# Performance work log

Hardware: AMD Instinct MI355X
Metric: run time of the kernel (lower is better)

Reference implementation:

```python
import jax, jax.numpy as jnp
import numpy as np

SQ3 = 3.0 ** 0.5

# ---- Clebsch-Gordan (real-basis Wigner 3j) constants, e3nn conventions ----
# e3nn real SH basis: polar axis = y, m=-l..l, azimuthal cos->z, sin->x,
# l=1 component order (x, y, z). Tensors normalized to unit Frobenius norm
# (e3nn wigner_3j normalization); overall sign is absorbed by random weights.

def _m2_basis():
    # symmetric traceless 3x3 matrices M_k with x^T M_k x = Y2_k(x)
    M = np.zeros((5, 3, 3))
    M[0, 0, 2] = M[0, 2, 0] = SQ3 / 2          # sqrt(3) x z
    M[1, 0, 1] = M[1, 1, 0] = SQ3 / 2          # sqrt(3) x y
    M[2] = np.diag([-0.5, 1.0, -0.5])           # y^2 - (x^2+z^2)/2
    M[3, 1, 2] = M[3, 2, 1] = SQ3 / 2          # sqrt(3) y z
    M[4] = np.diag([-SQ3 / 2, 0.0, SQ3 / 2])    # (sqrt(3)/2)(z^2-x^2)
    return M

def _w3j_112():
    C = np.zeros((3, 3, 5))
    C[0, 2, 0] = C[2, 0, 0] = SQ3 / 2
    C[0, 1, 1] = C[1, 0, 1] = SQ3 / 2
    C[1, 1, 2] = 1.0; C[0, 0, 2] = -0.5; C[2, 2, 2] = -0.5
    C[1, 2, 3] = C[2, 1, 3] = SQ3 / 2
    C[2, 2, 4] = SQ3 / 2; C[0, 0, 4] = -SQ3 / 2
    return C / np.linalg.norm(C)

def _w3j_222():
    M = _m2_basis()
    C = np.zeros((5, 5, 5))
    for i in range(5):
        for j in range(5):
            P = 0.5 * (M[i] @ M[j] + M[j] @ M[i])
            P -= (np.trace(P) / 3.0) * np.eye(3)
            for k in range(5):
                C[i, j, k] = np.trace(P @ M[k]) / 1.5
    return C / np.linalg.norm(C)

W112 = jnp.asarray(_w3j_112(), dtype=jnp.float32)
W222 = jnp.asarray(_w3j_222(), dtype=jnp.float32)


def _sh_component(v):
    # e3nn spherical harmonics, normalize=False, normalization='component'
    x, y, z = v[:, 0], v[:, 1], v[:, 2]
    x2, y2, z2 = x * x, y * y, z * z
    sh1 = SQ3 * v  # [E,3]
    sh2 = (5.0 ** 0.5) * jnp.stack([
        SQ3 * x * z,
        SQ3 * x * y,
        y2 - 0.5 * (x2 + z2),
        SQ3 * y * z,
        (SQ3 / 2.0) * (z2 - x2),
    ], axis=-1)  # [E,5]
    # l=3 SH exist in irreps_sh but no tp1 instruction consumes them (mid has no l=3)
    return sh1, sh2


def _forward(x, pos, tp1_w0, tp1_w1, tp1_w2, w_0e2e, w_2e0e, w_1o1o, w_2e2e):
    N = x.shape[0]
    E = N // 2  # setup guarantees exactly N/2 True entries per mask
    from_idx = jnp.nonzero(x[:, 0] > 0.5, size=E, fill_value=0)[0]
    to_idx = jnp.nonzero(x[:, 1] > 0.5, size=E, fill_value=0)[0]
    edge_vec = pos[to_idx] - pos[from_idx]          # [E,3]
    nf = x[to_idx]                                   # [E,2]  (2x0e)
    sh1, sh2 = _sh_component(edge_vec)

    # tp1: FCTP(2x0e, sh, 64x0e+24x1e+24x1o+16x2e+16x2o).
    # Live paths: 0e x 0e -> 0e, 0e x 1o -> 1o, 0e x 2e -> 2e; each path's
    # sqrt(dim_out/2) norm coeff times w3j(0,l,l)=delta/sqrt(2l+1) nets 1/sqrt(2).
    # 1e and 2o mid channels are structurally zero.
    # Sum over edges then / sqrt(6) (num_neighbors**0.5), folded into `inv`.
    inv = 1.0 / (2.0 ** 0.5 * 6.0 ** 0.5)
    g0 = inv * jnp.sum(nf @ tp1_w0, axis=0)                   # [64]  (sh0 == 1)
    g1 = inv * jnp.einsum('ew,ej->wj', nf @ tp1_w1, sh1)      # [24,3]
    g2 = inv * jnp.einsum('ew,ej->wj', nf @ tp1_w2, sh2)      # [16,5]

    # tp2: FCTP(mid, mid, 1x2e). element path norm: alpha = 5 / sum(mul1*mul2)
    # over ALL 10 instructions targeting 2e = 5248 (dead paths still count).
    c = (5.0 / 5248.0) ** 0.5
    inv_s5 = 1.0 / 5.0 ** 0.5  # w3j(0,2,2) = delta / sqrt(5)
    out = c * (
        inv_s5 * jnp.einsum('uv,u,vk->k', w_0e2e, g0, g2)
        + inv_s5 * jnp.einsum('uv,uk,v->k', w_2e0e, g2, g0)
        + jnp.einsum('uv,ui,vj,ijk->k', w_1o1o, g1, g1, W112)
        + jnp.einsum('uv,ui,vj,ijk->k', w_2e2e, g2, g2, W222)
    )
    return out  # [5]  (1x2e)


def setup_inputs() -> dict:
    key = jax.random.key(0)
    ks = jax.random.split(key, 9)
    N = 2_000_000
    E = N // 2
    base = 0.49 * jax.random.uniform(ks[0], (N, 2), dtype=jnp.float32)
    is_from = (jnp.arange(N) < E).astype(jnp.float32)
    # first half of nodes: x[:,0] > 0.5 (edge sources); second half: x[:,1] > 0.5 (targets)
    x = base.at[:, 0].add(0.51 * is_from).at[:, 1].add(0.51 * (1.0 - is_from))
    pos = jax.random.normal(ks[1], (N, 3), dtype=jnp.float32)
    return {
        'x': x,
        'pos': pos,
        'tp1_w0': jax.random.normal(ks[2], (2, 64), dtype=jnp.float32),
        'tp1_w1': jax.random.normal(ks[3], (2, 24), dtype=jnp.float32),
        'tp1_w2': jax.random.normal(ks[4], (2, 16), dtype=jnp.float32),
        'w_0e2e': jax.random.normal(ks[5], (64, 16), dtype=jnp.float32),
        'w_2e0e': jax.random.normal(ks[6], (16, 64), dtype=jnp.float32),
        'w_1o1o': jax.random.normal(ks[7], (24, 24), dtype=jnp.float32),
        'w_2e2e': jax.random.normal(ks[8], (16, 16), dtype=jnp.float32),
    }


def reference(x, pos, tp1_w0, tp1_w1, tp1_w2, w_0e2e, w_2e0e, w_1o1o, w_2e2e):
    return _forward(x, pos, tp1_w0, tp1_w1, tp1_w2, w_0e2e, w_2e0e, w_1o1o, w_2e2e)
```

## Files before the change

### kernel.cpp

```cpp
#include <hip/hip_runtime.h>

#define SQ3F 1.7320508075688772f
#define SQ5F 2.2360679774997896f
#define BLOCK 256
#define CHUNK 2048
#define ROUNDS 8
#define EPB 1024

__device__ const float M2B[5][3][3] = {
  {{0.f, 0.f, 0.8660254037844386f}, {0.f, 0.f, 0.f}, {0.8660254037844386f, 0.f, 0.f}},
  {{0.f, 0.8660254037844386f, 0.f}, {0.8660254037844386f, 0.f, 0.f}, {0.f, 0.f, 0.f}},
  {{-0.5f, 0.f, 0.f}, {0.f, 1.0f, 0.f}, {0.f, 0.f, -0.5f}},
  {{0.f, 0.f, 0.f}, {0.f, 0.f, 0.8660254037844386f}, {0.f, 0.8660254037844386f, 0.f}},
  {{-0.8660254037844386f, 0.f, 0.f}, {0.f, 0.f, 0.f}, {0.f, 0.f, 0.8660254037844386f}}
};

__device__ __forceinline__ void accum18(float* s, float nx, float ny,
                                        float ex, float ey, float ez) {
  float x2 = ex * ex, y2 = ey * ey, z2 = ez * ez;
  float s1x = SQ3F * ex, s1y = SQ3F * ey, s1z = SQ3F * ez;
  float s20 = SQ5F * SQ3F * ex * ez;
  float s21 = SQ5F * SQ3F * ex * ey;
  float s22 = SQ5F * (y2 - 0.5f * (x2 + z2));
  float s23 = SQ5F * SQ3F * ey * ez;
  float s24 = SQ5F * 0.5f * SQ3F * (z2 - x2);
  s[0] += nx;        s[1] += ny;
  s[2] += nx * s1x;  s[3] += nx * s1y;  s[4] += nx * s1z;
  s[5] += ny * s1x;  s[6] += ny * s1y;  s[7] += ny * s1z;
  s[8]  += nx * s20; s[9]  += nx * s21; s[10] += nx * s22;
  s[11] += nx * s23; s[12] += nx * s24;
  s[13] += ny * s20; s[14] += ny * s21; s[15] += ny * s22;
  s[16] += ny * s23; s[17] += ny * s24;
}

__device__ __forceinline__ void block_reduce_store(float* s, float* dst) {
  const int t = threadIdx.x, lane = t & 63, wave = t >> 6;
#pragma unroll
  for (int j = 0; j < 18; ++j)
    for (int o = 32; o; o >>= 1) s[j] += __shfl_down(s[j], o);
  __shared__ float ls[4][18];
  if (lane == 0) {
#pragma unroll
    for (int j = 0; j < 18; ++j) ls[wave][j] = s[j];
  }
  __syncthreads();
  if (t < 18) dst[t] = ls[0][t] + ls[1][t] + ls[2][t] + ls[3][t];
}

__device__ void do_finalize(const float* accS,
                            const float* w0, const float* w1, const float* w2,
                            const float* w_0e2e, const float* w_2e0e,
                            const float* w_1o1o, const float* w_2e2e,
                            float* out) {
  const int t = threadIdx.x;
  __shared__ float g0[64], g1[24][3], g2[16][5];
  __shared__ float a16[16], c16[16], T1[24][3], T2[16][5];
  __shared__ float A1[3][3], A2[5][5];
  __shared__ float W112s[45], W222s[125];
  __shared__ float rn112, rn222;
  if (t >= 64 && t < 109) W112s[t - 64] = 0.f;
  __syncthreads();

  const float inv = 0.28867513459481287f;
  if (t < 64) {
    g0[t] = inv * (accS[0] * w0[t] + accS[1] * w0[64 + t]);
  } else if (t < 136) {
    int i2 = t - 64, w = i2 / 3, j = i2 % 3;
    g1[w][j] = inv * (accS[2 + j] * w1[w] + accS[5 + j] * w1[24 + w]);
  } else if (t < 216) {
    int i2 = t - 136, w = i2 / 5, j = i2 % 5;
    g2[w][j] = inv * (accS[8 + j] * w2[w] + accS[13 + j] * w2[16 + w]);
  } else if (t < 241) {
    int idx = t - 216, i = idx / 5, j = idx % 5;
    float P[3][3];
    for (int a = 0; a < 3; ++a)
      for (int bb = 0; bb < 3; ++bb) {
        float sacc = 0.f;
        for (int cc = 0; cc < 3; ++cc)
          sacc += M2B[i][a][cc] * M2B[j][cc][bb] + M2B[j][a][cc] * M2B[i][cc][bb];
        P[a][bb] = 0.5f * sacc;
      }
    float tr3 = (P[0][0] + P[1][1] + P[2][2]) * (1.0f / 3.0f);
    P[0][0] -= tr3; P[1][1] -= tr3; P[2][2] -= tr3;
    for (int k = 0; k < 5; ++k) {
      float sacc = 0.f;
      for (int a = 0; a < 3; ++a)
        for (int bb = 0; bb < 3; ++bb) sacc += P[a][bb] * M2B[k][bb][a];
      W222s[(i * 5 + j) * 5 + k] = sacc * (1.0f / 1.5f);
    }
  }
  if (t == 0) {
    const float sq = 0.8660254037844386f;
    W112s[(0 * 3 + 2) * 5 + 0] = sq;  W112s[(2 * 3 + 0) * 5 + 0] = sq;
    W112s[(0 * 3 + 1) * 5 + 1] = sq;  W112s[(1 * 3 + 0) * 5 + 1] = sq;
    W112s[(1 * 3 + 1) * 5 + 2] = 1.0f;
    W112s[(0 * 3 + 0) * 5 + 2] = -0.5f;
    W112s[(2 * 3 + 2) * 5 + 2] = -0.5f;
    W112s[(1 * 3 + 2) * 5 + 3] = sq;  W112s[(2 * 3 + 1) * 5 + 3] = sq;
    W112s[(2 * 3 + 2) * 5 + 4] = sq;
    W112s[(0 * 3 + 0) * 5 + 4] = -sq;
  }
  __syncthreads();
  if (t == 0) { float ss = 0.f; for (int i = 0; i < 45; ++i)  ss += W112s[i] * W112s[i]; rn112 = rsqrtf(ss); }
  if (t == 1) { float ss = 0.f; for (int i = 0; i < 125; ++i) ss += W222s[i] * W222s[i]; rn222 = rsqrtf(ss); }
  __syncthreads();
  if (t < 45) W112s[t] *= rn112;
  else if (t < 170) W222s[t - 45] *= rn222;
  __syncthreads();

  if (t < 16) {
    float ssum = 0.f; for (int u = 0; u < 64; ++u) ssum += w_0e2e[u * 16 + t] * g0[u];
    a16[t] = ssum;
  } else if (t < 32) {
    int u = t - 16; float ssum = 0.f;
    for (int v = 0; v < 64; ++v) ssum += w_2e0e[u * 64 + v] * g0[v];
    c16[u] = ssum;
  } else if (t < 104) {
    int i2 = t - 32, u = i2 / 3, j = i2 % 3; float ssum = 0.f;
    for (int v = 0; v < 24; ++v) ssum += w_1o1o[u * 24 + v] * g1[v][j];
    T1[u][j] = ssum;
  } else if (t < 184) {
    int i2 = t - 104, u = i2 / 5, j = i2 % 5; float ssum = 0.f;
    for (int v = 0; v < 16; ++v) ssum += w_2e2e[u * 16 + v] * g2[v][j];
    T2[u][j] = ssum;
  }
  __syncthreads();
  if (t < 9) {
    int i = t / 3, j = t % 3; float ssum = 0.f;
    for (int u = 0; u < 24; ++u) ssum += g1[u][i] * T1[u][j];
    A1[i][j] = ssum;
  } else if (t < 34) {
    int i2 = t - 9, i = i2 / 5, j = i2 % 5; float ssum = 0.f;
    for (int u = 0; u < 16; ++u) ssum += g2[u][i] * T2[u][j];
    A2[i][j] = ssum;
  }
  __syncthreads();
  if (t < 5) {
    const float inv_s5 = 0.4472135954999579f;
    const float c = sqrtf(5.0f / 5248.0f);
    float s12 = 0.f;
    for (int v = 0; v < 16; ++v) s12 += (a16[v] + c16[v]) * g2[v][t];
    float s3 = 0.f;
    for (int i = 0; i < 3; ++i)
      for (int j = 0; j < 3; ++j) s3 += A1[i][j] * W112s[(i * 3 + j) * 5 + t];
    float s4 = 0.f;
    for (int i = 0; i < 5; ++i)
      for (int j = 0; j < 5; ++j) s4 += A2[i][j] * W222s[(i * 5 + j) * 5 + t];
    out[t] = c * (inv_s5 * s12 + s3 + s4);
  }
}

__global__ void __launch_bounds__(BLOCK)
spec_kernel(const float2* __restrict__ x, const float* __restrict__ pos,
            int N, int E, int nchunks,
            int* __restrict__ counts, int* __restrict__ canon,
            unsigned short* __restrict__ slabF, unsigned short* __restrict__ slabT,
            float* __restrict__ partials, int* __restrict__ done) {
  const int b = blockIdx.x, t = threadIdx.x;
  const int lane = t & 63, wave = t >> 6;
  const int chunkBase = b * CHUNK;
  if (b == 0 && t == 0) *done = 0;

  int ok = 1;
  for (int r = 0; r < ROUNDS; ++r) {
    int i = chunkBase + r * BLOCK + t;
    bool mf = false, mt = false;
    if (i < N) { float2 v = x[i]; mf = v.x > 0.5f; mt = v.y > 0.5f; }
    ok &= (int)((mf == (i < E)) && (mt == ((i >= E) && (i < N))));
  }
  ok = __all(ok) ? 1 : 0;
  __shared__ int okW[4];
  if (lane == 0) okW[wave] = ok;
  __syncthreads();
  const int chunkCanon = okW[0] & okW[1] & okW[2] & okW[3];

  if (chunkCanon) {
    if (t == 0) {
      int hi = chunkBase + CHUNK; if (hi > N) hi = N;
      int span = hi - chunkBase; if (span < 0) span = 0;
      int lf = E - chunkBase; if (lf < 0) lf = 0; if (lf > span) lf = span;
      counts[2 * b] = lf; counts[2 * b + 1] = span - lf;
      canon[b] = 1;
    }
  } else {
    __shared__ int wc[2][4][2];
    unsigned short* sF = slabF + (size_t)b * CHUNK;
    unsigned short* sT = slabT + (size_t)b * CHUNK;
    int localF = 0, localT = 0;
    for (int r = 0; r < ROUNDS; ++r) {
      const int li = r * BLOCK + t;
      const int i = chunkBase + li;
      bool mf = false, mt = false;
      if (i < N) { float2 v = x[i]; mf = v.x > 0.5f; mt = v.y > 0.5f; }
      unsigned long long bf = __ballot(mf);
      unsigned long long bt = __ballot(mt);
      const int p = r & 1;
      if (lane == 0) { wc[p][wave][0] = __popcll(bf); wc[p][wave][1] = __popcll(bt); }
      __syncthreads();
      int woF = 0, woT = 0, rtF = 0, rtT = 0;
      for (int w = 0; w < 4; ++w) {
        int a = wc[p][w][0], c = wc[p][w][1];
        if (w < wave) { woF += a; woT += c; }
        rtF += a; rtT += c;
      }
      unsigned long long lm = (1ull << lane) - 1ull;
      if (mf) sF[localF + woF + (int)__popcll(bf & lm)] = (unsigned short)li;
      if (mt) sT[localT + woT + (int)__popcll(bt & lm)] = (unsigned short)li;
      localF += rtF; localT += rtT;
    }
    if (t == 0) {
      counts[2 * b] = localF; counts[2 * b + 1] = localT;
      canon[b] = 0;
    }
  }

  float s[18];
#pragma unroll
  for (int j = 0; j < 18; ++j) s[j] = 0.f;
  const int k0 = b * EPB;
  if (k0 < E) {
    int k1 = k0 + EPB; if (k1 > E) k1 = E;
    if (((E & 3) == 0)) {
      int k = k0 + 4 * t;
      if (k + 4 <= k1) {
        const int g = k >> 2;
        const float4* pF4 = (const float4*)pos;
        const float4* pT4 = (const float4*)(pos + 3 * (size_t)E);
        const float4* xT4 = (const float4*)((const float*)x + 2 * (size_t)E);
        float4 fa = pF4[3 * g], fb = pF4[3 * g + 1], fc = pF4[3 * g + 2];
        float4 ta = pT4[3 * g], tb = pT4[3 * g + 1], tc = pT4[3 * g + 2];
        float4 xa = xT4[2 * g], xb = xT4[2 * g + 1];
        accum18(s, xa.x, xa.y, ta.x - fa.x, ta.y - fa.y, ta.z - fa.z);
        accum18(s, xa.z, xa.w, ta.w - fa.w, tb.x - fb.x, tb.y - fb.y);
        accum18(s, xb.x, xb.y, tb.z - fb.z, tb.w - fb.w, tc.x - fc.x);
        accum18(s, xb.z, xb.w, tc.y - fc.y, tc.z - fc.z, tc.w - fc.w);
      } else {
        for (int kk = k; kk < k1; ++kk) {
          float2 nf = x[E + kk];
          accum18(s, nf.x, nf.y,
                  pos[3 * (size_t)(E + kk)]     - pos[3 * (size_t)kk],
                  pos[3 * (size_t)(E + kk) + 1] - pos[3 * (size_t)kk + 1],
                  pos[3 * (size_t)(E + kk) + 2] - pos[3 * (size_t)kk + 2]);
        }
      }
    } else {
      for (int k = k0 + t; k < k1; k += BLOCK) {
        float2 nf = x[E + k];
        accum18(s, nf.x, nf.y,
                pos[3 * (size_t)(E + k)]     - pos[3 * (size_t)k],
                pos[3 * (size_t)(E + k) + 1] - pos[3 * (size_t)k + 1],
                pos[3 * (size_t)(E + k) + 2] - pos[3 * (size_t)k + 2]);
      }
    }
  }
  __syncthreads();
  block_reduce_store(s, partials + (size_t)b * 18);
}

__global__ void __launch_bounds__(BLOCK)
resolve_kernel(const float2* __restrict__ x, const float* __restrict__ pos,
               const int* __restrict__ counts, const int* __restrict__ canon,
               int nchunks, int E,
               const unsigned short* __restrict__ slabF,
               const unsigned short* __restrict__ slabT,
               float* __restrict__ partials, int* __restrict__ done,
               const float* __restrict__ w0, const float* __restrict__ w1,
               const float* __restrict__ w2, const float* __restrict__ w_0e2e,
               const float* __restrict__ w_2e0e, const float* __restrict__ w_1o1o,
               const float* __restrict__ w_2e2e, float* __restrict__ out) {
  const int b = blockIdx.x, t = threadIdx.x;
  const int lane = t & 63, wave = t >> 6;
  __shared__ float accS[18];

  int myok = 1;
  for (int k = t; k < nchunks; k += BLOCK) myok &= canon[k];
  myok = __all(myok) ? 1 : 0;
  __shared__ int cr[4];
  if (lane == 0) cr[wave] = myok;
  __syncthreads();
  const int allCanon = cr[0] & cr[1] & cr[2] & cr[3];

  if (allCanon) {
    if (b != 0) return;
    float s[18];
#pragma unroll
    for (int j = 0; j < 18; ++j) s[j] = 0.f;
    for (int p = t; p < nchunks; p += BLOCK) {
#pragma unroll
      for (int j = 0; j < 18; ++j) s[j] += partials[(size_t)p * 18 + j];
    }
    __syncthreads();
    block_reduce_store(s, accS);
    do_finalize(accS, w0, w1, w2, w_0e2e, w_2e0e, w_1o1o, w_2e2e, out);
    return;
  }

  __shared__ int pf[1025], pt[1025];
  __shared__ char cs[1024];
  for (int k = t; k < 1024; k += BLOCK) {
    pf[k] = (k < nchunks) ? counts[2 * k]     : 0;
    pt[k] = (k < nchunks) ? counts[2 * k + 1] : 0;
    cs[k] = (k < nchunks) ? (char)canon[k]    : (char)1;
  }
  __syncthreads();
  int a0 = pf[4 * t], a1 = pf[4 * t + 1], a2 = pf[4 * t + 2], a3 = pf[4 * t + 3];
  int b0 = pt[4 * t], b1 = pt[4 * t + 1], b2 = pt[4 * t + 2], b3 = pt[4 * t + 3];
  int sA = a0 + a1 + a2 + a3, sB = b0 + b1 + b2 + b3;
  int vA = sA, vB = sB;
  for (int o = 1; o < 64; o <<= 1) {
    int uA = __shfl_up(vA, o), uB = __shfl_up(vB, o);
    if (lane >= o) { vA += uA; vB += uB; }
  }
  __shared__ int wtA[4], wtB[4];
  if (lane == 63) { wtA[wave] = vA; wtB[wave] = vB; }
  __syncthreads();
  int woA = 0, woB = 0;
  for (int w = 0; w < wave; ++w) { woA += wtA[w]; woB += wtB[w]; }
  const int exA = vA - sA + woA;
  const int exB = vB - sB + woB;
  __syncthreads();
  pf[4 * t] = exA; pf[4 * t + 1] = exA + a0; pf[4 * t + 2] = exA + a0 + a1; pf[4 * t + 3] = exA + a0 + a1 + a2;
  pt[4 * t] = exB; pt[4 * t + 1] = exB + b0; pt[4 * t + 2] = exB + b0 + b1; pt[4 * t + 3] = exB + b0 + b1 + b2;
  if (t == BLOCK - 1) { pf[1024] = exA + sA; pt[1024] = exB + sB; }
  __syncthreads();

  int cF = pf[nchunks]; if (cF > E) cF = E;
  int cT = pt[nchunks]; if (cT > E) cT = E;

  float s[18];
#pragma unroll
  for (int j = 0; j < 18; ++j) s[j] = 0.f;
  const int k0 = b * EPB;
  int k1 = k0 + EPB; if (k1 > E) k1 = E;
  for (int k = k0 + t; k < k1; k += BLOCK) {
    int idxF = 0, idxT = 0;
    if (k < cF) {
      int lo = 0, hi = nchunks - 1;
      while (lo < hi) { int mid = (lo + hi) >> 1; if (pf[mid + 1] <= k) lo = mid + 1; else hi = mid; }
      int loc = k - pf[lo];
      idxF = lo * CHUNK + (cs[lo] ? loc : (int)slabF[(size_t)lo * CHUNK + loc]);
    }
    if (k < cT) {
      int lo = 0, hi = nchunks - 1;
      while (lo < hi) { int mid = (lo + hi) >> 1; if (pt[mid + 1] <= k) lo = mid + 1; else hi = mid; }
      int loc = k - pt[lo];
      int startT = pf[lo + 1] - pf[lo];
      idxT = lo * CHUNK + (cs[lo] ? (startT + loc) : (int)slabT[(size_t)lo * CHUNK + loc]);
    }
    float2 nf = x[idxT];
    float ex = pos[3 * (size_t)idxT]     - pos[3 * (size_t)idxF];
    float ey = pos[3 * (size_t)idxT + 1] - pos[3 * (size_t)idxF + 1];
    float ez = pos[3 * (size_t)idxT + 2] - pos[3 * (size_t)idxF + 2];
    accum18(s, nf.x, nf.y, ex, ey, ez);
  }
  __syncthreads();
  block_reduce_store(s, partials + (size_t)b * 18);
  __threadfence();
  __shared__ int lastFlag;
  if (t == 0) lastFlag = (atomicAdd(done, 1) == (int)gridDim.x - 1) ? 1 : 0;
  __syncthreads();
  if (!lastFlag) return;
  __threadfence();
  float s2[18];
#pragma unroll
  for (int j = 0; j < 18; ++j) s2[j] = 0.f;
  for (int p = t; p < nchunks; p += BLOCK) {
#pragma unroll
    for (int j = 0; j < 18; ++j) s2[j] += partials[(size_t)p * 18 + j];
  }
  __syncthreads();
  block_reduce_store(s2, accS);
  do_finalize(accS, w0, w1, w2, w_0e2e, w_2e0e, w_1o1o, w_2e2e, out);
}

extern "C" void kernel_launch(void* const* d_in, const int* in_sizes, int n_in,
                              void* d_out, int out_size, void* d_ws, size_t ws_size,
                              hipStream_t stream) {
  const float2* x      = (const float2*)d_in[0];
  const float*  pos    = (const float*)d_in[1];
  const float*  tp1_w0 = (const float*)d_in[2];
  const float*  tp1_w1 = (const float*)d_in[3];
  const float*  tp1_w2 = (const float*)d_in[4];
  const float*  w_0e2e = (const float*)d_in[5];
  const float*  w_2e0e = (const float*)d_in[6];
  const float*  w_1o1o = (const float*)d_in[7];
  const float*  w_2e2e = (const float*)d_in[8];
  float* outp = (float*)d_out;

  const int N = in_sizes[0] / 2;
  const int E = N / 2;
  const int nchunks = (N + CHUNK - 1) / CHUNK;

  char* ws = (char*)d_ws;
  int*   done     = (int*)ws;
  int*   counts   = (int*)(ws + 128);
  int*   canon    = (int*)(ws + 128 + 8192);
  float* partials = (float*)(ws + 128 + 8192 + 4096);
  unsigned short* slabF = (unsigned short*)(ws + 128 + 8192 + 4096 + 73728);
  unsigned short* slabT = slabF + (size_t)nchunks * CHUNK;

  spec_kernel<<<nchunks, BLOCK, 0, stream>>>(x, pos, N, E, nchunks, counts, canon,
                                             slabF, slabT, partials, done);
  resolve_kernel<<<nchunks, BLOCK, 0, stream>>>(x, pos, counts, canon, nchunks, E,
                                                slabF, slabT, partials, done,
                                                tp1_w0, tp1_w1, tp1_w2,
                                                w_0e2e, w_2e0e, w_1o1o, w_2e2e, outp);
}
```

Baseline: 26.79 us.

## Fold mask canonicality check into edge pass and use single-block fallback

The separate chunk scan of x is removed. Each edge block now checks the from/to mask pattern on the rows it already reads (plus a vectorized read of the first-half x rows) and records a per-block canonical flag. The second kernel becomes a single block that either reduces partials on the fast path or, if any block is non-canonical, does a serial compaction and accumulation over all nodes. This drops the slab-writing and the large multi-block resolve launch from the common path. In exchange the fallback is far slower, since one block now processes two million nodes.

After: 24.25 us. 9.5% less time.

```diff
diff --git a/kernel.cpp b/kernel.cpp
--- a/kernel.cpp
+++ b/kernel.cpp
@@ -3,8 +3,6 @@
 #define SQ3F 1.7320508075688772f
 #define SQ5F 2.2360679774997896f
 #define BLOCK 256
-#define CHUNK 2048
-#define ROUNDS 8
 #define EPB 1024
 
 __device__ const float M2B[5][3][3] = {
@@ -152,75 +150,34 @@
 
 __global__ void __launch_bounds__(BLOCK)
 spec_kernel(const float2* __restrict__ x, const float* __restrict__ pos,
-            int N, int E, int nchunks,
-            int* __restrict__ counts, int* __restrict__ canon,
-            unsigned short* __restrict__ slabF, unsigned short* __restrict__ slabT,
-            float* __restrict__ partials, int* __restrict__ done) {
+            int N, int E,
+            int* __restrict__ canon, float* __restrict__ partials) {
   const int b = blockIdx.x, t = threadIdx.x;
   const int lane = t & 63, wave = t >> 6;
-  const int chunkBase = b * CHUNK;
-  if (b == 0 && t == 0) *done = 0;
+  const int k0 = b * EPB;
+  int k1 = k0 + EPB; if (k1 > E) k1 = E;
 
   int ok = 1;
-  for (int r = 0; r < ROUNDS; ++r) {
-    int i = chunkBase + r * BLOCK + t;
-    bool mf = false, mt = false;
-    if (i < N) { float2 v = x[i]; mf = v.x > 0.5f; mt = v.y > 0.5f; }
-    ok &= (int)((mf == (i < E)) && (mt == ((i >= E) && (i < N))));
-  }
-  ok = __all(ok) ? 1 : 0;
-  __shared__ int okW[4];
-  if (lane == 0) okW[wave] = ok;
-  __syncthreads();
-  const int chunkCanon = okW[0] & okW[1] & okW[2] & okW[3];
-
-  if (chunkCanon) {
-    if (t == 0) {
-      int hi = chunkBase + CHUNK; if (hi > N) hi = N;
-      int span = hi - chunkBase; if (span < 0) span = 0;
-      int lf = E - chunkBase; if (lf < 0) lf = 0; if (lf > span) lf = span;
-      counts[2 * b] = lf; counts[2 * b + 1] = span - lf;
-      canon[b] = 1;
-    }
-  } else {
-    __shared__ int wc[2][4][2];
-    unsigned short* sF = slabF + (size_t)b * CHUNK;
-    unsigned short* sT = slabT + (size_t)b * CHUNK;
-    int localF = 0, localT = 0;
-    for (int r = 0; r < ROUNDS; ++r) {
-      const int li = r * BLOCK + t;
-      const int i = chunkBase + li;
-      bool mf = false, mt = false;
-      if (i < N) { float2 v = x[i]; mf = v.x > 0.5f; mt = v.y > 0.5f; }
-      unsigned long long bf = __ballot(mf);
-      unsigned long long bt = __ballot(mt);
-      const int p = r & 1;
-      if (lane == 0) { wc[p][wave][0] = __popcll(bf); wc[p][wave][1] = __popcll(bt); }
-      __syncthreads();
-      int woF = 0, woT = 0, rtF = 0, rtT = 0;
-      for (int w = 0; w < 4; ++w) {
-        int a = wc[p][w][0], c = wc[p][w][1];
-        if (w < wave) { woF += a; woT += c; }
-        rtF += a; rtT += c;
-      }
-      unsigned long long lm = (1ull << lane) - 1ull;
-      if (mf) sF[localF + woF + (int)__popcll(bf & lm)] = (unsigned short)li;
-      if (mt) sT[localT + woT + (int)__popcll(bt & lm)] = (unsigned short)li;
-      localF += rtF; localT += rtT;
-    }
-    if (t == 0) {
-      counts[2 * b] = localF; counts[2 * b + 1] = localT;
-      canon[b] = 0;
-    }
-  }
-
   float s[18];
 #pragma unroll
   for (int j = 0; j < 18; ++j) s[j] = 0.f;
-  const int k0 = b * EPB;
+
   if (k0 < E) {
-    int k1 = k0 + EPB; if (k1 > E) k1 = E;
-    if (((E & 3) == 0)) {
+    {
+      const float4* x4 = (const float4*)x;
+      const int nrows = k1 - k0;
+      const int n4 = nrows >> 1;
+      for (int q = t; q < n4; q += BLOCK) {
+        float4 v = x4[(k0 >> 1) + q];
+        ok &= (int)(v.x > 0.5f) & (int)!(v.y > 0.5f)
+            & (int)(v.z > 0.5f) & (int)!(v.w > 0.5f);
+      }
+      if ((nrows & 1) && t == 0) {
+        float2 v = x[k1 - 1];
+        ok &= (int)(v.x > 0.5f) & (int)!(v.y > 0.5f);
+      }
+    }
+    if ((E & 3) == 0) {
       int k = k0 + 4 * t;
       if (k + 4 <= k1) {
         const int g = k >> 2;
@@ -230,6 +187,10 @@
         float4 fa = pF4[3 * g], fb = pF4[3 * g + 1], fc = pF4[3 * g + 2];
         float4 ta = pT4[3 * g], tb = pT4[3 * g + 1], tc = pT4[3 * g + 2];
         float4 xa = xT4[2 * g], xb = xT4[2 * g + 1];
+        ok &= (int)!(xa.x > 0.5f) & (int)(xa.y > 0.5f)
+            & (int)!(xa.z > 0.5f) & (int)(xa.w > 0.5f)
+            & (int)!(xb.x > 0.5f) & (int)(xb.y > 0.5f)
+            & (int)!(xb.z > 0.5f) & (int)(xb.w > 0.5f);
         accum18(s, xa.x, xa.y, ta.x - fa.x, ta.y - fa.y, ta.z - fa.z);
         accum18(s, xa.z, xa.w, ta.w - fa.w, tb.x - fb.x, tb.y - fb.y);
         accum18(s, xb.x, xb.y, tb.z - fb.z, tb.w - fb.w, tc.x - fc.x);
@@ -237,6 +198,7 @@
       } else {
         for (int kk = k; kk < k1; ++kk) {
           float2 nf = x[E + kk];
+          ok &= (int)!(nf.x > 0.5f) & (int)(nf.y > 0.5f);
           accum18(s, nf.x, nf.y,
                   pos[3 * (size_t)(E + kk)]     - pos[3 * (size_t)kk],
                   pos[3 * (size_t)(E + kk) + 1] - pos[3 * (size_t)kk + 1],
@@ -246,6 +208,7 @@
     } else {
       for (int k = k0 + t; k < k1; k += BLOCK) {
         float2 nf = x[E + k];
+        ok &= (int)!(nf.x > 0.5f) & (int)(nf.y > 0.5f);
         accum18(s, nf.x, nf.y,
                 pos[3 * (size_t)(E + k)]     - pos[3 * (size_t)k],
                 pos[3 * (size_t)(E + k) + 1] - pos[3 * (size_t)k + 1],
@@ -253,39 +216,42 @@
       }
     }
   }
-  __syncthreads();
+
+  ok = __all(ok) ? 1 : 0;
+  __shared__ int okW[4];
+  if (lane == 0) okW[wave] = ok;
+  __syncthreads();
+  if (t == 0) canon[b] = okW[0] & okW[1] & okW[2] & okW[3];
+
   block_reduce_store(s, partials + (size_t)b * 18);
 }
 
 __global__ void __launch_bounds__(BLOCK)
-resolve_kernel(const float2* __restrict__ x, const float* __restrict__ pos,
-               const int* __restrict__ counts, const int* __restrict__ canon,
-               int nchunks, int E,
-               const unsigned short* __restrict__ slabF,
-               const unsigned short* __restrict__ slabT,
-               float* __restrict__ partials, int* __restrict__ done,
-               const float* __restrict__ w0, const float* __restrict__ w1,
-               const float* __restrict__ w2, const float* __restrict__ w_0e2e,
-               const float* __restrict__ w_2e0e, const float* __restrict__ w_1o1o,
-               const float* __restrict__ w_2e2e, float* __restrict__ out) {
-  const int b = blockIdx.x, t = threadIdx.x;
+finalize_kernel(const float2* __restrict__ x, const float* __restrict__ pos,
+                const int* __restrict__ canon, int nb, int N, int E,
+                const float* __restrict__ partials,
+                int* __restrict__ fromList, int* __restrict__ toList,
+                const float* __restrict__ w0, const float* __restrict__ w1,
+                const float* __restrict__ w2, const float* __restrict__ w_0e2e,
+                const float* __restrict__ w_2e0e, const float* __restrict__ w_1o1o,
+                const float* __restrict__ w_2e2e, float* __restrict__ out) {
+  const int t = threadIdx.x;
   const int lane = t & 63, wave = t >> 6;
   __shared__ float accS[18];
+  __shared__ int cr[4];
 
   int myok = 1;
-  for (int k = t; k < nchunks; k += BLOCK) myok &= canon[k];
+  for (int k = t; k < nb; k += BLOCK) myok &= canon[k];
   myok = __all(myok) ? 1 : 0;
-  __shared__ int cr[4];
   if (lane == 0) cr[wave] = myok;
   __syncthreads();
   const int allCanon = cr[0] & cr[1] & cr[2] & cr[3];
 
   if (allCanon) {
-    if (b != 0) return;
     float s[18];
 #pragma unroll
     for (int j = 0; j < 18; ++j) s[j] = 0.f;
-    for (int p = t; p < nchunks; p += BLOCK) {
+    for (int p = t; p < nb; p += BLOCK) {
 #pragma unroll
       for (int j = 0; j < 18; ++j) s[j] += partials[(size_t)p * 18 + j];
     }
@@ -295,81 +261,47 @@
     return;
   }
 
-  __shared__ int pf[1025], pt[1025];
-  __shared__ char cs[1024];
-  for (int k = t; k < 1024; k += BLOCK) {
-    pf[k] = (k < nchunks) ? counts[2 * k]     : 0;
-    pt[k] = (k < nchunks) ? counts[2 * k + 1] : 0;
-    cs[k] = (k < nchunks) ? (char)canon[k]    : (char)1;
-  }
-  __syncthreads();
-  int a0 = pf[4 * t], a1 = pf[4 * t + 1], a2 = pf[4 * t + 2], a3 = pf[4 * t + 3];
-  int b0 = pt[4 * t], b1 = pt[4 * t + 1], b2 = pt[4 * t + 2], b3 = pt[4 * t + 3];
-  int sA = a0 + a1 + a2 + a3, sB = b0 + b1 + b2 + b3;
-  int vA = sA, vB = sB;
-  for (int o = 1; o < 64; o <<= 1) {
-    int uA = __shfl_up(vA, o), uB = __shfl_up(vB, o);
-    if (lane >= o) { vA += uA; vB += uB; }
-  }
-  __shared__ int wtA[4], wtB[4];
-  if (lane == 63) { wtA[wave] = vA; wtB[wave] = vB; }
-  __syncthreads();
-  int woA = 0, woB = 0;
-  for (int w = 0; w < wave; ++w) { woA += wtA[w]; woB += wtB[w]; }
-  const int exA = vA - sA + woA;
-  const int exB = vB - sB + woB;
-  __syncthreads();
-  pf[4 * t] = exA; pf[4 * t + 1] = exA + a0; pf[4 * t + 2] = exA + a0 + a1; pf[4 * t + 3] = exA + a0 + a1 + a2;
-  pt[4 * t] = exB; pt[4 * t + 1] = exB + b0; pt[4 * t + 2] = exB + b0 + b1; pt[4 * t + 3] = exB + b0 + b1 + b2;
-  if (t == BLOCK - 1) { pf[1024] = exA + sA; pt[1024] = exB + sB; }
-  __syncthreads();
-
-  int cF = pf[nchunks]; if (cF > E) cF = E;
-  int cT = pt[nchunks]; if (cT > E) cT = E;
+  __shared__ int wc[2][4][2];
+  int cF = 0, cT = 0;
+  const int iters = (N + BLOCK - 1) / BLOCK;
+  for (int r = 0; r < iters; ++r) {
+    const int i = r * BLOCK + t;
+    bool mf = false, mt = false;
+    if (i < N) { float2 v = x[i]; mf = v.x > 0.5f; mt = v.y > 0.5f; }
+    unsigned long long bf = __ballot(mf);
+    unsigned long long bt = __ballot(mt);
+    const int p = r & 1;
+    if (lane == 0) { wc[p][wave][0] = __popcll(bf); wc[p][wave][1] = __popcll(bt); }
+    __syncthreads();
+    int woF = 0, woT = 0, rtF = 0, rtT = 0;
+    for (int w = 0; w < 4; ++w) {
+      int a = wc[p][w][0], c = wc[p][w][1];
+      if (w < wave) { woF += a; woT += c; }
+      rtF += a; rtT += c;
+    }
+    unsigned long long lm = (1ull << lane) - 1ull;
+    if (mf) { int rk = cF + woF + (int)__popcll(bf & lm); if (rk < E) fromList[rk] = i; }
+    if (mt) { int rk = cT + woT + (int)__popcll(bt & lm); if (rk < E) toList[rk] = i; }
+    cF += rtF; cT += rtT;
+  }
+  __syncthreads();
+  int limF = cF < E ? cF : E;
+  int limT = cT < E ? cT : E;
 
   float s[18];
 #pragma unroll
   for (int j = 0; j < 18; ++j) s[j] = 0.f;
-  const int k0 = b * EPB;
-  int k1 = k0 + EPB; if (k1 > E) k1 = E;
-  for (int k = k0 + t; k < k1; k += BLOCK) {
-    int idxF = 0, idxT = 0;
-    if (k < cF) {
-      int lo = 0, hi = nchunks - 1;
-      while (lo < hi) { int mid = (lo + hi) >> 1; if (pf[mid + 1] <= k) lo = mid + 1; else hi = mid; }
-      int loc = k - pf[lo];
-      idxF = lo * CHUNK + (cs[lo] ? loc : (int)slabF[(size_t)lo * CHUNK + loc]);
-    }
-    if (k < cT) {
-      int lo = 0, hi = nchunks - 1;
-      while (lo < hi) { int mid = (lo + hi) >> 1; if (pt[mid + 1] <= k) lo = mid + 1; else hi = mid; }
-      int loc = k - pt[lo];
-      int startT = pf[lo + 1] - pf[lo];
-      idxT = lo * CHUNK + (cs[lo] ? (startT + loc) : (int)slabT[(size_t)lo * CHUNK + loc]);
-    }
-    float2 nf = x[idxT];
-    float ex = pos[3 * (size_t)idxT]     - pos[3 * (size_t)idxF];
-    float ey = pos[3 * (size_t)idxT + 1] - pos[3 * (size_t)idxF + 1];
-    float ez = pos[3 * (size_t)idxT + 2] - pos[3 * (size_t)idxF + 2];
-    accum18(s, nf.x, nf.y, ex, ey, ez);
-  }
-  __syncthreads();
-  block_reduce_store(s, partials + (size_t)b * 18);
-  __threadfence();
-  __shared__ int lastFlag;
-  if (t == 0) lastFlag = (atomicAdd(done, 1) == (int)gridDim.x - 1) ? 1 : 0;
-  __syncthreads();
-  if (!lastFlag) return;
-  __threadfence();
-  float s2[18];
-#pragma unroll
-  for (int j = 0; j < 18; ++j) s2[j] = 0.f;
-  for (int p = t; p < nchunks; p += BLOCK) {
-#pragma unroll
-    for (int j = 0; j < 18; ++j) s2[j] += partials[(size_t)p * 18 + j];
-  }
-  __syncthreads();
-  block_reduce_store(s2, accS);
+  for (int k = t; k < E; k += BLOCK) {
+    int f  = (k < limF) ? fromList[k] : 0;
+    int tt = (k < limT) ? toList[k]   : 0;
+    float2 nf = x[tt];
+    accum18(s, nf.x, nf.y,
+            pos[3 * (size_t)tt]     - pos[3 * (size_t)f],
+            pos[3 * (size_t)tt + 1] - pos[3 * (size_t)f + 1],
+            pos[3 * (size_t)tt + 2] - pos[3 * (size_t)f + 2]);
+  }
+  __syncthreads();
+  block_reduce_store(s, accS);
   do_finalize(accS, w0, w1, w2, w_0e2e, w_2e0e, w_1o1o, w_2e2e, out);
 }
 
@@ -389,20 +321,18 @@
 
   const int N = in_sizes[0] / 2;
   const int E = N / 2;
-  const int nchunks = (N + CHUNK - 1) / CHUNK;
+  int nb = (E + EPB - 1) / EPB;
+  if (nb < 1) nb = 1;
 
   char* ws = (char*)d_ws;
-  int*   done     = (int*)ws;
-  int*   counts   = (int*)(ws + 128);
-  int*   canon    = (int*)(ws + 128 + 8192);
-  float* partials = (float*)(ws + 128 + 8192 + 4096);
-  unsigned short* slabF = (unsigned short*)(ws + 128 + 8192 + 4096 + 73728);
-  unsigned short* slabT = slabF + (size_t)nchunks * CHUNK;
-
-  spec_kernel<<<nchunks, BLOCK, 0, stream>>>(x, pos, N, E, nchunks, counts, canon,
-                                             slabF, slabT, partials, done);
-  resolve_kernel<<<nchunks, BLOCK, 0, stream>>>(x, pos, counts, canon, nchunks, E,
-                                                slabF, slabT, partials, done,
-                                                tp1_w0, tp1_w1, tp1_w2,
-                                                w_0e2e, w_2e0e, w_1o1o, w_2e2e, outp);
-}
+  int*   canon    = (int*)ws;
+  float* partials = (float*)(ws + 4096);
+  int*   fromList = (int*)(ws + 4096 + 73728);
+  int*   toList   = fromList + E;
+
+  spec_kernel<<<nb, BLOCK, 0, stream>>>(x, pos, N, E, canon, partials);
+  finalize_kernel<<<1, BLOCK, 0, stream>>>(x, pos, canon, nb, N, E, partials,
+                                           fromList, toList,
+                                           tp1_w0, tp1_w1, tp1_w2,
+                                           w_0e2e, w_2e0e, w_1o1o, w_2e2e, outp);
+}
```
